# Kernel tuning notes

Hardware: AMD Instinct MI355X
Metric: run time of the kernel (lower is better)

The kernel has to match this reference:

```python
import jax, jax.numpy as jnp
from jax import lax
import numpy as np

DG = 8          # deformable_groups
NF = 64         # num_feat
K = 3
KK = K * K


def conv3(x, w, b):
    # 3x3 'same' conv, NCHW / OIHW
    return lax.conv_general_dilated(x, w, (1, 1), 'SAME',
                                    dimension_numbers=('NCHW', 'OIHW', 'NCHW')) + b[None, :, None, None]


def deform_conv(x, offset, w, b, dg=DG):
    # Offset-only deformable conv (DCN), 3x3, stride 1, pad 1.
    # x: (B,C,H,W); offset: (B, dg*KK*2, H, W) ordered (group, kernel_pos, [dy,dx])
    B, C, H, W = x.shape
    Cg = C // dg
    dt = x.dtype
    off = offset.reshape(B, dg, KK, 2, H, W)
    gy = jnp.arange(H, dtype=dt)[:, None]                      # (H,1)
    gx = jnp.arange(W, dtype=dt)[None, :]                      # (1,W)
    ky = (jnp.arange(KK) // K - 1).astype(dt)[:, None, None]   # (KK,1,1)
    kx = (jnp.arange(KK) % K - 1).astype(dt)[:, None, None]
    py = gy + ky + off[:, :, :, 0]                             # (B,dg,KK,H,W)
    px = gx + kx + off[:, :, :, 1]
    xg = x.reshape(B, dg, Cg, H, W)

    def sample(img, py, px):
        # img (Cg,H,W); py,px (KK,H,W) -> (Cg,KK,H,W); zero padding outside image
        y0 = jnp.floor(py); x0 = jnp.floor(px)
        wy = py - y0; wx = px - x0
        y0 = y0.astype(jnp.int32); x0 = x0.astype(jnp.int32)
        imf = img.reshape(Cg, H * W)

        def gather(yi, xi):
            valid = ((yi >= 0) & (yi < H) & (xi >= 0) & (xi < W)).astype(dt)
            flat = (jnp.clip(yi, 0, H - 1) * W + jnp.clip(xi, 0, W - 1)).reshape(-1)
            return imf[:, flat].reshape(Cg, KK, H, W) * valid

        v00 = gather(y0, x0);     v01 = gather(y0, x0 + 1)
        v10 = gather(y0 + 1, x0); v11 = gather(y0 + 1, x0 + 1)
        return (v00 * (1 - wy) * (1 - wx) + v01 * (1 - wy) * wx
                + v10 * wy * (1 - wx) + v11 * wy * wx)

    samp = jax.vmap(jax.vmap(sample))(xg, py, px)   # (B,dg,Cg,KK,H,W)
    wr = w.reshape(-1, dg, Cg, KK)                  # (Cout,dg,Cg,KK) from (Cout,Cin,3,3)
    out = jnp.einsum('bgckhw,ogck->bohw', samp, wr)
    return out + b[None, :, None, None]


def _forward(pf, xc, cr_w, cr_b, off1_w, off1_b, dc1_w, dc1_b, off2_w, off2_b,
             dc2_w, dc2_b, off3_w, off3_b, dc3_w, dc3_b, off4_w, off4_b,
             dc4_w, dc4_b, rec_w, rec_b):
    B, N, C, H, W = pf.shape
    center = N // 2
    ref = pf[:, center]
    ys = []
    for i in range(N):  # N is a small static frame count (5)
        if i == center:
            ys.append(xc[:, None])
            continue
        supp = pf[:, i]
        fea = conv3(jnp.concatenate([ref, supp], axis=1), cr_w, cr_b)
        fea = deform_conv(fea, conv3(fea, off1_w, off1_b), dc1_w, dc1_b)
        fea = deform_conv(fea, conv3(fea, off2_w, off2_b), dc2_w, dc2_b)
        fea = deform_conv(supp, conv3(fea, off3_w, off3_b), dc3_w, dc3_b)
        aligned = deform_conv(fea, conv3(fea, off4_w, off4_b), dc4_w, dc4_b)
        ys.append(conv3(aligned, rec_w, rec_b)[:, None])
    return jnp.concatenate(ys, axis=1)  # (B, N, 3, H, W)


def setup_inputs() -> dict:
    key = jax.random.key(0)
    ks = jax.random.split(key, 16)
    B, N, C, H, W = 2, 5, NF, 128, 128
    offc = 18 * DG

    def cw(k, cout, cin):
        # matches init_weights: normal(0, sqrt(2 / (k*k*out_channels)))
        return jax.random.normal(k, (cout, cin, 3, 3), jnp.float32) * float(np.sqrt(2.0 / (9 * cout)))

    return {
        'precomputed_features': jax.random.normal(ks[0], (B, N, C, H, W), jnp.float32),
        'x_center': jax.random.normal(ks[1], (B, 3, H, W), jnp.float32),
        'cr_w': cw(ks[2], C, 2 * C), 'cr_b': jnp.zeros((C,), jnp.float32),
        'off1_w': cw(ks[3], offc, C), 'off1_b': jnp.zeros((offc,), jnp.float32),
        'dc1_w': cw(ks[4], C, C), 'dc1_b': jnp.zeros((C,), jnp.float32),
        'off2_w': cw(ks[5], offc, C), 'off2_b': jnp.zeros((offc,), jnp.float32),
        'dc2_w': cw(ks[6], C, C), 'dc2_b': jnp.zeros((C,), jnp.float32),
        'off3_w': cw(ks[7], offc, C), 'off3_b': jnp.zeros((offc,), jnp.float32),
        'dc3_w': cw(ks[8], C, C), 'dc3_b': jnp.zeros((C,), jnp.float32),
        'off4_w': cw(ks[9], offc, C), 'off4_b': jnp.zeros((offc,), jnp.float32),
        'dc4_w': cw(ks[10], C, C), 'dc4_b': jnp.zeros((C,), jnp.float32),
        'rec_w': cw(ks[11], 3, C), 'rec_b': jnp.zeros((3,), jnp.float32),
    }


def reference(precomputed_features, x_center, cr_w, cr_b, off1_w, off1_b, dc1_w, dc1_b,
              off2_w, off2_b, dc2_w, dc2_b, off3_w, off3_b, dc3_w, dc3_b,
              off4_w, off4_b, dc4_w, dc4_b, rec_w, rec_b):
    return _forward(precomputed_features, x_center, cr_w, cr_b, off1_w, off1_b, dc1_w, dc1_b,
                    off2_w, off2_b, dc2_w, dc2_b, off3_w, off3_b, dc3_w, dc3_b,
                    off4_w, off4_b, dc4_w, dc4_b, rec_w, rec_b)
```

## Files before the change

kernel.cpp:

```cpp
#include <hip/hip_runtime.h>

#define HH 128
#define WW 128
#define HWP (HH*WW)
#define NC 64
#define NB 2
#define NN 5
#define OFFC 144
#define NKC 18

typedef __attribute__((ext_vector_type(8))) _Float16 half8;
typedef __attribute__((ext_vector_type(4))) float floatx4;
typedef __attribute__((ext_vector_type(2))) float floatx2;

__global__ __launch_bounds__(256) void copy_center_k(const float* __restrict__ xc,
                                                     float* __restrict__ out) {
    int idx = blockIdx.x * 256 + threadIdx.x;
    const int total = NB * 3 * HWP;
    if (idx >= total) return;
    int b = idx / (3 * HWP);
    int r = idx - b * 3 * HWP;
    out[(size_t)((b * NN + 2) * 3) * HWP + r] = xc[idx];
}

__global__ __launch_bounds__(256) void repack_k(const float* __restrict__ pf,
                                                float* __restrict__ dst, int job0, int is_ref)
{
    __shared__ float T[64][65];
    const int jl = blockIdx.y;
    const float* src;
    if (is_ref) {
        src = pf + (size_t)((jl * NN + 2) * NC) * HWP;
    } else {
        int jg = job0 + jl;
        int b = jg & 1, fi = jg >> 1;
        int frame = fi + (fi >= 2 ? 1 : 0);
        src = pf + (size_t)((b * NN + frame) * NC) * HWP;
    }
    float* d = dst + (size_t)jl * NC * HWP;
    const int p0 = blockIdx.x * 64;
    const int tid = threadIdx.x;
    const int lx = tid & 63, cg4 = tid >> 6;
#pragma unroll
    for (int cc = 0; cc < 16; ++cc) {
        int c = cc * 4 + cg4;
        T[c][lx] = src[(size_t)c * HWP + p0 + lx];
    }
    __syncthreads();
    const int px = tid >> 2, c0 = (tid & 3) * 16;
#pragma unroll
    for (int j = 0; j < 4; ++j) {
        floatx4 v = { T[c0 + j*4 + 0][px], T[c0 + j*4 + 1][px],
                      T[c0 + j*4 + 2][px], T[c0 + j*4 + 3][px] };
        *(floatx4*)(d + (size_t)(p0 + px) * 64 + c0 + j*4) = v;
    }
}

__global__ __launch_bounds__(256) void prew_k(const float* __restrict__ w,
                                              _Float16* __restrict__ wp,
                                              int nct, int nkc, int mode,
                                              int ci_off, int cin_src)
{
    int idx = blockIdx.x * 256 + threadIdx.x;
    if (idx >= nct * nkc * 64) return;
    int lane = idx & 63;
    int kc = (idx >> 6) % nkc;
    int ct = (idx >> 6) / nkc;
    int m = lane & 15, quad = lane >> 4;
    int co = ct * 16 + m;
    union { half8 v; _Float16 e[8]; } ph, pl;
#pragma unroll
    for (int j = 0; j < 8; ++j) {
        int k = kc * 32 + quad * 8 + j;
        float f = 0.f;
        if (mode == 0) {
            int kk = k >> 6, ci = k & 63;
            f = w[((size_t)co * cin_src + ci_off + ci) * 9 + kk];
        } else {
            int r = k / 160, kr = k - r * 160;
            if (kr < 144) {
                int g = r * 2 + kr / 72;
                int rr = kr % 72;
                int kk = rr >> 3, cg = rr & 7;
                f = w[((size_t)co * cin_src + g * 8 + cg) * 9 + kk];
            }
        }
        _Float16 h = (_Float16)f;
        ph.e[j] = h; pl.e[j] = (_Float16)(f - (float)h);
    }
    size_t base = (size_t)((ct * nkc + kc) * 2) * 512;
    *(half8*)(wp + base + lane * 8) = ph.v;
    *(half8*)(wp + base + 512 + lane * 8) = pl.v;
}

template<int NCT, int SRCMODE, int ADD>
__global__ __launch_bounds__(256, 3) void mconv_k(
    const float* __restrict__ src, const float* __restrict__ R,
    const float* __restrict__ S, const _Float16* __restrict__ wp,
    const float* __restrict__ bias, float* __restrict__ out, int job0)
{
    constexpr int PL = 1456;
    constexpr int Ct = NCT * 16;
    const int jl = blockIdx.y, jg = job0 + jl;
    const int b = jg & 1;
    const int tile = blockIdx.x;
    const int ty0 = (tile >> 3) << 3, tx0 = (tile & 7) << 4;
    const int tid = threadIdx.x;
    const int lane = tid & 63;
    const int wq = __builtin_amdgcn_readfirstlane(tid >> 6);
    const int n = lane & 15, quad = lane >> 4;

    const float* s0;
    if (SRCMODE == 0)      s0 = src + (size_t)jl * NC * HWP;
    else if (SRCMODE == 1) s0 = R + (size_t)b * NC * HWP;
    else                   s0 = S + (size_t)jl * NC * HWP;

    __shared__ _Float16 hh[8 * PL];
    __shared__ _Float16 ll[8 * PL];

    for (int t = tid; t < 360; t += 256) {
        int px = t >> 1, hf = t & 1;
        int hy = px / 18, hx = px - hy * 18;
        int gy = ty0 - 1 + hy, gx = tx0 - 1 + hx;
        bool ok = (gy >= 0 && gy < HH && gx >= 0 && gx < WW);
        const float* sp = s0 + (ok ? ((size_t)(gy * WW + gx) * 64) : 0) + hf * 32;
        int lb = px * 8;
#pragma unroll
        for (int c = 0; c < 4; ++c) {
            int cb = hf * 4 + c;
            floatx4 f0 = {0.f,0.f,0.f,0.f}, f1 = {0.f,0.f,0.f,0.f};
            if (ok) {
                f0 = *(const floatx4*)(sp + c * 8);
                f1 = *(const floatx4*)(sp + c * 8 + 4);
            }
            union { half8 v; _Float16 e[8]; } ph, pl;
#pragma unroll
            for (int j = 0; j < 4; ++j) {
                _Float16 h0 = (_Float16)f0[j], h1 = (_Float16)f1[j];
                ph.e[j] = h0;     ph.e[j+4] = h1;
                pl.e[j] = (_Float16)(f0[j] - (float)h0);
                pl.e[j+4] = (_Float16)(f1[j] - (float)h1);
            }
            *(half8*)&hh[cb * PL + lb] = ph.v;
            *(half8*)&ll[cb * PL + lb] = pl.v;
        }
    }
    __syncthreads();

    floatx4 acc0[NCT], acc1[NCT];
#pragma unroll
    for (int ct = 0; ct < NCT; ++ct) {
        acc0[ct] = floatx4{0.f, 0.f, 0.f, 0.f};
        acc1[ct] = floatx4{0.f, 0.f, 0.f, 0.f};
    }
    const int y0 = wq * 2, y1 = y0 + 1;
#pragma unroll
    for (int kc = 0; kc < NKC; ++kc) {
        const int kk = kc >> 1;
        const int dy = kk / 3, dx = kk % 3;
        const int cb = ((kc & 1) << 2) + quad;
        const int ix0 = cb * PL + ((y0 + dy) * 18 + n + dx) * 8;
        const int ix1 = cb * PL + ((y1 + dy) * 18 + n + dx) * 8;
        half8 B0h = *(const half8*)&hh[ix0];
        half8 B0l = *(const half8*)&ll[ix0];
        half8 B1h = *(const half8*)&hh[ix1];
        half8 B1l = *(const half8*)&ll[ix1];
        const _Float16* wk = wp + (size_t)kc * 1024 + lane * 8;
#pragma unroll
        for (int ct = 0; ct < NCT; ++ct) {
            const _Float16* wc = wk + (size_t)ct * NKC * 1024;
            half8 Ah = *(const half8*)wc;
            half8 Al = *(const half8*)(wc + 512);
            acc0[ct] = __builtin_amdgcn_mfma_f32_16x16x32_f16(Ah, B0h, acc0[ct], 0, 0, 0);
            acc0[ct] = __builtin_amdgcn_mfma_f32_16x16x32_f16(Ah, B0l, acc0[ct], 0, 0, 0);
            acc0[ct] = __builtin_amdgcn_mfma_f32_16x16x32_f16(Al, B0h, acc0[ct], 0, 0, 0);
            acc1[ct] = __builtin_amdgcn_mfma_f32_16x16x32_f16(Ah, B1h, acc1[ct], 0, 0, 0);
            acc1[ct] = __builtin_amdgcn_mfma_f32_16x16x32_f16(Ah, B1l, acc1[ct], 0, 0, 0);
            acc1[ct] = __builtin_amdgcn_mfma_f32_16x16x32_f16(Al, B1h, acc1[ct], 0, 0, 0);
        }
    }

    const int oy0 = ty0 + y0, oy1 = ty0 + y1, ox = tx0 + n;
#pragma unroll
    for (int ct = 0; ct < NCT; ++ct) {
        const floatx4 b4 = *(const floatx4*)(bias + ct * 16 + quad * 4);
        float* op0 = out + ((size_t)jl * HWP + (size_t)oy0 * WW + ox) * Ct
                         + ct * 16 + quad * 4;
        float* op1 = out + ((size_t)jl * HWP + (size_t)oy1 * WW + ox) * Ct
                         + ct * 16 + quad * 4;
        floatx4 v0 = acc0[ct], v1 = acc1[ct];
        if (ADD) {
            v0 += *(const floatx4*)op0;
            v1 += *(const floatx4*)op1;
        } else {
            v0 += b4;
            v1 += b4;
        }
        *(floatx4*)op0 = v0;
        *(floatx4*)op1 = v1;
    }
}

__global__ __launch_bounds__(512, 6) void mdeform_k(
    const float* __restrict__ in, const float* __restrict__ off,
    const _Float16* __restrict__ wp, const float* __restrict__ bias,
    float* __restrict__ out, int supp_mode, const float* __restrict__ S)
{
    constexpr int SROW = 166;
    const int jl = blockIdx.y;
    const int tile = blockIdx.x;
    const int ty0 = (tile >> 4) << 3, tx0 = (tile & 15) << 3;
    const int tid = threadIdx.x;
    const int lane = tid & 63;
    const int w8 = __builtin_amdgcn_readfirstlane(tid >> 6);
    const int q = w8 >> 1;
    const int sb2 = (w8 & 1) << 1;
    const int n = lane & 15, quad = lane >> 4;

    const float* ibase = supp_mode ? (S + (size_t)jl * NC * HWP)
                                   : (in + (size_t)jl * NC * HWP);
    const float* obase = off + (size_t)jl * OFFC * HWP;

    __shared__ _Float16 sh[64 * SROW];
    __shared__ _Float16 sl[64 * SROW];

    for (int e = tid; e < 64 * 16; e += 512) {
        int row = e >> 4, col = 144 + (e & 15);
        sh[row * SROW + col] = (_Float16)0.f;
        sl[row * SROW + col] = (_Float16)0.f;
    }

    floatx4 acc[2];
#pragma unroll
    for (int s = 0; s < 2; ++s) acc[s] = floatx4{0.f, 0.f, 0.f, 0.f};

    for (int r = 0; r < 4; ++r) {
        __syncthreads();
        for (int i = 0; i < 5; ++i) {
            int idx = tid + (i << 9);
            if (idx >= 2304) break;
            int hf = idx & 1;
            int pair = idx >> 1;
            int gl = pair / 576;
            int rem = pair - gl * 576;
            int kk = rem >> 6;
            int px = rem & 63;
            int g = r * 2 + gl;
            int yy = ty0 + (px >> 3), xx = tx0 + (px & 7);
            floatx2 o2 = *(const floatx2*)(obase + (size_t)(yy * WW + xx) * OFFC
                                           + (g * 9 + kk) * 2);
            float pyf = (float)(yy + (kk / 3) - 1) + o2[0];
            float pxf = (float)(xx + (kk % 3) - 1) + o2[1];
            float fy = floorf(pyf), fx = floorf(pxf);
            float wy = pyf - fy, wx = pxf - fx;
            int y0 = (int)fy, x0 = (int)fx;
            int y1 = y0 + 1, x1 = x0 + 1;
            float m00 = (y0 >= 0 && y0 < HH && x0 >= 0 && x0 < WW) ? 1.f : 0.f;
            float m01 = (y0 >= 0 && y0 < HH && x1 >= 0 && x1 < WW) ? 1.f : 0.f;
            float m10 = (y1 >= 0 && y1 < HH && x0 >= 0 && x0 < WW) ? 1.f : 0.f;
            float m11 = (y1 >= 0 && y1 < HH && x1 >= 0 && x1 < WW) ? 1.f : 0.f;
            float w00 = (1.f - wy) * (1.f - wx) * m00;
            float w01 = (1.f - wy) * wx * m01;
            float w10 = wy * (1.f - wx) * m10;
            float w11 = wy * wx * m11;
            int cy0 = min(max(y0, 0), HH - 1), cy1 = min(max(y1, 0), HH - 1);
            int cx0 = min(max(x0, 0), WW - 1), cx1 = min(max(x1, 0), WW - 1);
            const int co = g * 8 + hf * 4;
            const float* p00 = ibase + (size_t)(cy0 * WW + cx0) * 64 + co;
            const float* p01 = ibase + (size_t)(cy0 * WW + cx1) * 64 + co;
            const float* p10 = ibase + (size_t)(cy1 * WW + cx0) * 64 + co;
            const float* p11 = ibase + (size_t)(cy1 * WW + cx1) * 64 + co;
            floatx4 a = *(const floatx4*)p00;
            floatx4 b = *(const floatx4*)p01;
            floatx4 c = *(const floatx4*)p10;
            floatx4 d = *(const floatx4*)p11;
            floatx4 sv = a * w00 + b * w01 + c * w10 + d * w11;
            union { unsigned u[2]; _Float16 e[4]; } P, L;
#pragma unroll
            for (int j = 0; j < 4; ++j) {
                _Float16 h = (_Float16)sv[j];
                P.e[j] = h;
                L.e[j] = (_Float16)(sv[j] - (float)h);
            }
            int sb = px * SROW + gl * 72 + kk * 8 + hf * 4;
            unsigned* shp = (unsigned*)&sh[sb];
            unsigned* slp = (unsigned*)&sl[sb];
            shp[0] = P.u[0]; shp[1] = P.u[1];
            slp[0] = L.u[0]; slp[1] = L.u[1];
        }
        __syncthreads();
#pragma unroll
        for (int kc5 = 0; kc5 < 5; ++kc5) {
            int kcg = r * 5 + kc5;
            size_t base = (size_t)((q * 20 + kcg) * 2) * 512;
            half8 Ah = *(const half8*)(wp + base + lane * 8);
            half8 Al = *(const half8*)(wp + base + 512 + lane * 8);
#pragma unroll
            for (int s = 0; s < 2; ++s) {
                int px = (sb2 + s) * 16 + n;
                const int ix = px * SROW + kc5 * 32 + quad * 8;
                half8 Bh = *(const half8*)&sh[ix];
                half8 Bl = *(const half8*)&sl[ix];
                acc[s] = __builtin_amdgcn_mfma_f32_16x16x32_f16(Ah, Bh, acc[s], 0, 0, 0);
                acc[s] = __builtin_amdgcn_mfma_f32_16x16x32_f16(Ah, Bl, acc[s], 0, 0, 0);
                acc[s] = __builtin_amdgcn_mfma_f32_16x16x32_f16(Al, Bh, acc[s], 0, 0, 0);
            }
        }
    }
    const floatx4 b4 = *(const floatx4*)(bias + q * 16 + quad * 4);
#pragma unroll
    for (int s = 0; s < 2; ++s) {
        int px = (sb2 + s) * 16 + n;
        int oy = ty0 + (px >> 3), ox = tx0 + (px & 7);
        float* op = out + ((size_t)jl * HWP + (size_t)oy * WW + ox) * 64
                        + q * 16 + quad * 4;
        *(floatx4*)op = acc[s] + b4;
    }
}

__global__ __launch_bounds__(256) void conv3x3_rec_k(
    const float* __restrict__ in, const float* __restrict__ w,
    const float* __restrict__ bias, float* __restrict__ out, int job0)
{
    constexpr int CB = 8;
    constexpr int PITCH = 48;
    constexpr int CH = 18 * PITCH;
    const int jl = blockIdx.y, jg = job0 + jl;
    const int b = jg & 1, fi = jg >> 1;
    const int frame = fi + (fi >= 2 ? 1 : 0);
    const int tile = blockIdx.x;
    const int ty0 = (tile >> 3) << 4, tx0 = (tile & 7) << 4;
    const int tid = threadIdx.x;
    const int tx = tid & 15, ty = tid >> 4;
    const float* srcA = in + (size_t)jl * NC * HWP;

    __shared__ float lds[CB * CH];
    float acc[3] = {bias[0], bias[1], bias[2]};

    for (int cb = 0; cb < NC; cb += CB) {
        __syncthreads();
        for (int e = tid; e < CB * 324; e += 256) {
            int c = e & 7;
            int r = e >> 3;
            int iy = r / 18, ix = r - iy * 18;
            int gy = ty0 - 1 + iy, gx = tx0 - 1 + ix;
            float v = 0.f;
            if (gy >= 0 && gy < HH && gx >= 0 && gx < WW)
                v = srcA[(size_t)(gy * WW + gx) * 64 + cb + c];
            lds[c * CH + iy * PITCH + ix] = v;
        }
        __syncthreads();
#pragma unroll
        for (int c = 0; c < CB; ++c) {
            float t[9];
#pragma unroll
            for (int dy = 0; dy < 3; ++dy)
#pragma unroll
                for (int dx = 0; dx < 3; ++dx)
                    t[dy * 3 + dx] = lds[c * CH + (ty + dy) * PITCH + (tx + dx)];
            int ci = cb + c;
#pragma unroll
            for (int o = 0; o < 3; ++o) {
                const float* wo = w + ((size_t)o * NC + ci) * 9;
#pragma unroll
                for (int kk = 0; kk < 9; ++kk)
                    acc[o] = fmaf(wo[kk], t[kk], acc[o]);
            }
        }
    }
    const int oy = ty0 + ty, ox = tx0 + tx;
#pragma unroll
    for (int o = 0; o < 3; ++o)
        out[((size_t)(b * NN + frame) * 3 + o) * HWP + oy * WW + ox] = acc[o];
}

extern "C" void kernel_launch(void* const* d_in, const int* in_sizes, int n_in,
                              void* d_out, int out_size, void* d_ws, size_t ws_size,
                              hipStream_t stream)
{
    const float* pf    = (const float*)d_in[0];
    const float* xc    = (const float*)d_in[1];
    const float* cr_w  = (const float*)d_in[2];
    const float* cr_b  = (const float*)d_in[3];
    const float* ow[4] = {(const float*)d_in[4],  (const float*)d_in[8],
                          (const float*)d_in[12], (const float*)d_in[16]};
    const float* ob[4] = {(const float*)d_in[5],  (const float*)d_in[9],
                          (const float*)d_in[13], (const float*)d_in[17]};
    const float* dw[4] = {(const float*)d_in[6],  (const float*)d_in[10],
                          (const float*)d_in[14], (const float*)d_in[18]};
    const float* db[4] = {(const float*)d_in[7],  (const float*)d_in[11],
                          (const float*)d_in[15], (const float*)d_in[19]};
    const float* rec_w = (const float*)d_in[20];
    const float* rec_b = (const float*)d_in[21];
    float* out = (float*)d_out;

    const size_t WPC = (size_t)4 * NKC * 1024;
    const size_t WPO = (size_t)9 * NKC * 1024;
    const size_t WPD = (size_t)4 * 20 * 1024;
    _Float16* wp_cr0 = (_Float16*)d_ws;
    _Float16* wp_cr1 = wp_cr0 + WPC;
    _Float16* wp_of[4];
    _Float16* wp_dc[4];
    _Float16* curh = wp_cr1 + WPC;
    for (int i = 0; i < 4; ++i) { wp_of[i] = curh; curh += WPO; }
    for (int i = 0; i < 4; ++i) { wp_dc[i] = curh; curh += WPD; }
    size_t wp_bytes = (size_t)((char*)curh - (char*)d_ws);

    const size_t fplane = (size_t)NC * HWP;
    const size_t oplane = (size_t)OFFC * HWP;
    int JC = 8;
    while (JC > 1 &&
           wp_bytes + (2 + 3 * (size_t)JC) * fplane * 4 + (size_t)JC * oplane * 4 > ws_size)
        JC >>= 1;
    float* R  = (float*)curh;
    float* S  = R  + 2 * fplane;
    float* A  = S  + (size_t)JC * fplane;
    float* Bb = A  + (size_t)JC * fplane;
    float* O  = Bb + (size_t)JC * fplane;

    {
        int nc4 = 4 * NKC * 64, nc9 = 9 * NKC * 64, ncd = 4 * 20 * 64;
        dim3 b4((nc4 + 255) / 256), b9((nc9 + 255) / 256), bd((ncd + 255) / 256);
        prew_k<<<b4, 256, 0, stream>>>(cr_w, wp_cr0, 4, NKC, 0, 0, 128);
        prew_k<<<b4, 256, 0, stream>>>(cr_w, wp_cr1, 4, NKC, 0, 64, 128);
        for (int i = 0; i < 4; ++i) {
            prew_k<<<b9, 256, 0, stream>>>(ow[i], wp_of[i], 9, NKC, 0, 0, 64);
            prew_k<<<bd, 256, 0, stream>>>(dw[i], wp_dc[i], 4, 20, 1, 0, 64);
        }
        repack_k<<<dim3(256, 2), 256, 0, stream>>>(pf, R, 0, 1);
    }

    copy_center_k<<<dim3((NB * 3 * HWP + 255) / 256), 256, 0, stream>>>(xc, out);

    for (int job0 = 0; job0 < 8; job0 += JC) {
        dim3 blk(256);
        dim3 blk512(512);
        dim3 gconv(128, JC), gdef(256, JC), grec(64, JC);
        repack_k<<<dim3(256, JC), blk, 0, stream>>>(pf, S, job0, 0);
        mconv_k<4, 1, 0><<<gconv, blk, 0, stream>>>(nullptr, R, S, wp_cr0, cr_b, A, job0);
        mconv_k<4, 2, 1><<<gconv, blk, 0, stream>>>(nullptr, R, S, wp_cr1, cr_b, A, job0);
        mconv_k<9, 0, 0><<<gconv, blk, 0, stream>>>(A, R, S, wp_of[0], ob[0], O, job0);
        mdeform_k<<<gdef, blk512, 0, stream>>>(A, O, wp_dc[0], db[0], Bb, 0, S);
        mconv_k<9, 0, 0><<<gconv, blk, 0, stream>>>(Bb, R, S, wp_of[1], ob[1], O, job0);
        mdeform_k<<<gdef, blk512, 0, stream>>>(Bb, O, wp_dc[1], db[1], A, 0, S);
        mconv_k<9, 0, 0><<<gconv, blk, 0, stream>>>(A, R, S, wp_of[2], ob[2], O, job0);
        mdeform_k<<<gdef, blk512, 0, stream>>>(nullptr, O, wp_dc[2], db[2], Bb, 1, S);
        mconv_k<9, 0, 0><<<gconv, blk, 0, stream>>>(Bb, R, S, wp_of[3], ob[3], O, job0);
        mdeform_k<<<gdef, blk512, 0, stream>>>(Bb, O, wp_dc[3], db[3], A, 0, S);
        conv3x3_rec_k<<<grec, blk, 0, stream>>>(A, rec_w, rec_b, out, job0);
    }
}
```

Measured before the change: 1.294 ms.

## Stage input halo tile in LDS for deformable bilinear gathers

```diff
diff --git a/kernel.cpp b/kernel.cpp
--- a/kernel.cpp
+++ b/kernel.cpp
@@ -201,7 +201,7 @@
     }
 }
 
-__global__ __launch_bounds__(512, 6) void mdeform_k(
+__global__ __launch_bounds__(512, 4) void mdeform_k(
     const float* __restrict__ in, const float* __restrict__ off,
     const _Float16* __restrict__ wp, const float* __restrict__ bias,
     float* __restrict__ out, int supp_mode, const float* __restrict__ S)
@@ -213,7 +213,7 @@
     const int tid = threadIdx.x;
     const int lane = tid & 63;
     const int w8 = __builtin_amdgcn_readfirstlane(tid >> 6);
-    const int q = w8 >> 1;
+    const int q4 = w8 >> 1;
     const int sb2 = (w8 & 1) << 1;
     const int n = lane & 15, quad = lane >> 4;
 
@@ -223,6 +223,7 @@
 
     __shared__ _Float16 sh[64 * SROW];
     __shared__ _Float16 sl[64 * SROW];
+    __shared__ float stg[256 * 16];
 
     for (int e = tid; e < 64 * 16; e += 512) {
         int row = e >> 4, col = 144 + (e & 15);
@@ -235,6 +236,19 @@
     for (int s = 0; s < 2; ++s) acc[s] = floatx4{0.f, 0.f, 0.f, 0.f};
 
     for (int r = 0; r < 4; ++r) {
+#pragma unroll
+        for (int j = 0; j < 2; ++j) {
+            int t = tid + (j << 9);
+            int slot = t >> 2;
+            int qq = t & 3;
+            int ry = slot >> 4, rx = slot & 15;
+            int gy = ty0 - 4 + ry, gx = tx0 - 4 + rx;
+            if ((unsigned)gy < (unsigned)HH && (unsigned)gx < (unsigned)WW) {
+                floatx4 v = *(const floatx4*)(ibase + (size_t)(gy * WW + gx) * 64
+                                              + r * 16 + qq * 4);
+                *(floatx4*)&stg[(slot << 4) + ((qq ^ ((slot >> 1) & 3)) << 2)] = v;
+            }
+        }
         __syncthreads();
         for (int i = 0; i < 5; ++i) {
             int idx = tid + (i << 9);
@@ -265,15 +279,26 @@
             float w11 = wy * wx * m11;
             int cy0 = min(max(y0, 0), HH - 1), cy1 = min(max(y1, 0), HH - 1);
             int cx0 = min(max(x0, 0), WW - 1), cx1 = min(max(x1, 0), WW - 1);
-            const int co = g * 8 + hf * 4;
-            const float* p00 = ibase + (size_t)(cy0 * WW + cx0) * 64 + co;
-            const float* p01 = ibase + (size_t)(cy0 * WW + cx1) * 64 + co;
-            const float* p10 = ibase + (size_t)(cy1 * WW + cx0) * 64 + co;
-            const float* p11 = ibase + (size_t)(cy1 * WW + cx1) * 64 + co;
-            floatx4 a = *(const floatx4*)p00;
-            floatx4 b = *(const floatx4*)p01;
-            floatx4 c = *(const floatx4*)p10;
-            floatx4 d = *(const floatx4*)p11;
+            const int qc = (gl << 1) + hf;
+            int ry0 = cy0 - ty0 + 4, ry1 = cy1 - ty0 + 4;
+            int rx0 = cx0 - tx0 + 4, rx1 = cx1 - tx0 + 4;
+            bool allin = ((unsigned)ry0 < 16u) & ((unsigned)ry1 < 16u) &
+                         ((unsigned)rx0 < 16u) & ((unsigned)rx1 < 16u);
+            floatx4 a, b, c, d;
+            if (allin) {
+                int s00 = (ry0 << 4) + rx0, s01 = (ry0 << 4) + rx1;
+                int s10 = (ry1 << 4) + rx0, s11 = (ry1 << 4) + rx1;
+                a = *(const floatx4*)&stg[(s00 << 4) + ((qc ^ ((s00 >> 1) & 3)) << 2)];
+                b = *(const floatx4*)&stg[(s01 << 4) + ((qc ^ ((s01 >> 1) & 3)) << 2)];
+                c = *(const floatx4*)&stg[(s10 << 4) + ((qc ^ ((s10 >> 1) & 3)) << 2)];
+                d = *(const floatx4*)&stg[(s11 << 4) + ((qc ^ ((s11 >> 1) & 3)) << 2)];
+            } else {
+                const int co = g * 8 + hf * 4;
+                a = *(const floatx4*)(ibase + (size_t)(cy0 * WW + cx0) * 64 + co);
+                b = *(const floatx4*)(ibase + (size_t)(cy0 * WW + cx1) * 64 + co);
+                c = *(const floatx4*)(ibase + (size_t)(cy1 * WW + cx0) * 64 + co);
+                d = *(const floatx4*)(ibase + (size_t)(cy1 * WW + cx1) * 64 + co);
+            }
             floatx4 sv = a * w00 + b * w01 + c * w10 + d * w11;
             union { unsigned u[2]; _Float16 e[4]; } P, L;
 #pragma unroll
@@ -292,7 +317,7 @@
 #pragma unroll
         for (int kc5 = 0; kc5 < 5; ++kc5) {
             int kcg = r * 5 + kc5;
-            size_t base = (size_t)((q * 20 + kcg) * 2) * 512;
+            size_t base = (size_t)((q4 * 20 + kcg) * 2) * 512;
             half8 Ah = *(const half8*)(wp + base + lane * 8);
             half8 Al = *(const half8*)(wp + base + 512 + lane * 8);
 #pragma unroll
@@ -307,13 +332,13 @@
             }
         }
     }
-    const floatx4 b4 = *(const floatx4*)(bias + q * 16 + quad * 4);
+    const floatx4 b4 = *(const floatx4*)(bias + q4 * 16 + quad * 4);
 #pragma unroll
     for (int s = 0; s < 2; ++s) {
         int px = (sb2 + s) * 16 + n;
         int oy = ty0 + (px >> 3), ox = tx0 + (px & 7);
         float* op = out + ((size_t)jl * HWP + (size_t)oy * WW + ox) * 64
-                        + q * 16 + quad * 4;
+                        + q4 * 16 + quad * 4;
         *(floatx4*)op = acc[s] + b4;
     }
 }
```

New measurement: 1.220 ms. -5.7%, faster.
